# Kernel optimization log

Hardware: AMD Instinct MI355X
Metric: run time of the kernel (lower is better)

## Reference

```python
import jax, jax.numpy as jnp
import numpy as np

DEPTH = 6

def sparsemax(z):
    # sparsemax over last axis (Martins & Astudillo 2016)
    z_sorted = -jnp.sort(-z, axis=-1)
    z_cum = jnp.cumsum(z_sorted, axis=-1)
    k = jnp.arange(1, z.shape[-1] + 1, dtype=z.dtype)
    support = k * z_sorted > z_cum - 1.0
    k_sup = jnp.sum(support, axis=-1, keepdims=True).astype(jnp.int32)
    tau_sum = jnp.take_along_axis(z_cum, k_sup - 1, axis=-1)
    tau = (tau_sum - 1.0) / k_sup.astype(z.dtype)
    return jnp.maximum(z - tau, 0.0)

def sparsemoid(x):
    return jnp.clip(0.5 * x + 0.5, 0.0, 1.0)

def make_bin_codes(depth):
    indices = jnp.arange(2 ** depth)
    offsets = 2 ** jnp.arange(depth)
    bin_codes = ((indices[None, :] // offsets[:, None]) % 2).astype(jnp.float32)
    return jnp.stack([bin_codes, 1.0 - bin_codes], axis=-1)  # [depth, 2^depth, 2]

def odste_forward(x, fsl, esl, thr, lt, resp, codes):
    # x: [B,J,D]; fsl: [n,t,J]; esl: [n,t,J,D]; thr/lt: [n,t]; resp: [n,c,D,2^t]
    fs = sparsemax(fsl)                               # [n,t,J]
    es = sparsemax(esl)                               # [n,t,J,D]
    sel = jnp.einsum('bjd,ntj->bntd', x, fs)          # feature selection
    sel = sel * jnp.sum(es, axis=2)[None]             # einsum 'bntd,ntjd->bntd'
    tl = (sel - thr[None, :, :, None]) * jnp.exp(-lt)[None, :, :, None]
    tl = jnp.stack([-tl, tl], axis=-1)                # [b,n,t,d,2]
    bins = sparsemoid(tl)
    bm = jnp.einsum('bntds,tcs->bntdc', bins, codes)  # [b,n,t,d,c]
    rw = jnp.prod(bm, axis=2)                         # [b,n,d,c]
    return jnp.einsum('bnds,ncds->bnd', rw, resp)     # [b,n,d]


def setup_inputs() -> dict:
    key = jax.random.key(0)
    B, D, n, t, c_tree = 64, 32, 128, DEPTH, 1
    Js = [64, 192, 320]
    ks = jax.random.split(key, 1 + 5 * len(Js))
    inp = {'x': jax.random.normal(ks[0], (B, Js[0], D), dtype=jnp.float32)}
    for i, J in enumerate(Js):
        k0, k1, k2, k3, k4 = ks[1 + 5 * i:6 + 5 * i]
        inp[f'fsl_{i}'] = jax.random.uniform(k0, (n, t, J), dtype=jnp.float32)
        inp[f'esl_{i}'] = jax.random.normal(k1, (n, t, J, D), dtype=jnp.float32)
        inp[f'thr_{i}'] = jax.random.normal(k2, (n, t), dtype=jnp.float32)
        inp[f'lt_{i}'] = jax.random.normal(k3, (n, t), dtype=jnp.float32)
        inp[f'resp_{i}'] = jax.random.normal(k4, (n, c_tree, D, 2 ** t), dtype=jnp.float32)
    return inp


def reference(x, fsl_0, esl_0, thr_0, lt_0, resp_0,
              fsl_1, esl_1, thr_1, lt_1, resp_1,
              fsl_2, esl_2, thr_2, lt_2, resp_2):
    codes = make_bin_codes(DEPTH)
    layers = [(fsl_0, esl_0, thr_0, lt_0, resp_0),
              (fsl_1, esl_1, thr_1, lt_1, resp_1),
              (fsl_2, esl_2, thr_2, lt_2, resp_2)]
    for fsl, esl, thr, lt, resp in layers:
        h = odste_forward(x, fsl, esl, thr, lt, resp, codes)
        x = jnp.concatenate([x, h], axis=1)
    return x
```

## Files before the change

### kernel.cpp

```cpp
#include <hip/hip_runtime.h>

#define OUT_COLS 448
#define OUT_STRIDE (OUT_COLS * 32)
#define NTREES 128
#define TDEPTH 6
#define NT (NTREES * TDEPTH)
#define DD 32
#define BB 64
#define PADW 64

template <int CTRL, int RMASK = 0xf, bool BC = true>
__device__ __forceinline__ float dppf(float v) {
    return __int_as_float(
        __builtin_amdgcn_update_dpp(0, __float_as_int(v), CTRL, RMASK, 0xf, BC));
}

__device__ __forceinline__ float wred64(float x) {
    x += dppf<0x111>(x);
    x += dppf<0x112>(x);
    x += dppf<0x114>(x);
    x += dppf<0x118>(x);
    x += __int_as_float(__builtin_amdgcn_update_dpp(0, __float_as_int(x), 0x142, 0xa, 0xf, false));
    x += __int_as_float(__builtin_amdgcn_update_dpp(0, __float_as_int(x), 0x143, 0xc, 0xf, false));
    return __int_as_float(__builtin_amdgcn_readlane(__float_as_int(x), 63));
}

template <int J>
__device__ __forceinline__ void fs_row(const float* __restrict__ zr, int lane,
                                       int* __restrict__ fj, float* __restrict__ fv,
                                       int* __restrict__ fcnt_p) {
    constexpr int T = J / 64;
    float z[T];
    #pragma unroll
    for (int t = 0; t < T; ++t) z[t] = zr[t * 64 + lane];
    float sp = 0.f;
    #pragma unroll
    for (int t = 0; t < T; ++t) sp += z[t];
    float k = (float)J;
    float tau = (wred64(sp) - 1.f) / k;
    #pragma unroll 1
    for (int it = 0; it < 64; ++it) {
        float s2 = 0.f, c2 = 0.f;
        #pragma unroll
        for (int t = 0; t < T; ++t) {
            bool g = z[t] > tau;
            s2 += g ? z[t] : 0.f;
            c2 += g ? 1.f : 0.f;
        }
        float S2 = wred64(s2);
        float K2 = wred64(c2);
        if (K2 == k) break;
        k = K2;
        tau = (S2 - 1.f) / K2;
    }
    unsigned long long below = (1ull << lane) - 1ull;
    int base = 0;
    #pragma unroll
    for (int t = 0; t < T; ++t) {
        bool sup = z[t] > tau;
        unsigned long long m = __ballot(sup);
        int pos = base + __popcll(m & below);
        if (sup && pos < PADW) { fj[pos] = t * 64 + lane; fv[pos] = z[t] - tau; }
        base += __popcll(m);
    }
    int cnt = base < PADW ? base : PADW;
    for (int i = cnt + lane; i < PADW; i += 64) { fj[i] = 0; fv[i] = 0.f; }
    if (lane == 0) *fcnt_p = cnt;
}

template <int S>
__device__ __forceinline__ void bstep(float* a, int lane) {
    constexpr int half = 16 >> S;
    bool up = ((lane >> S) & 1) != 0;
    #pragma unroll
    for (int q = 0; q < half; ++q) {
        float send = up ? a[q] : a[half + q];
        float recv;
        if constexpr (S == 0)      recv = dppf<0xB1>(send);
        else if constexpr (S == 1) recv = dppf<0x4E>(send);
        else recv = __int_as_float(__builtin_amdgcn_ds_swizzle(
                        __float_as_int(send), ((1 << S) << 10) | 0x1F));
        float keep = up ? a[half + q] : a[q];
        a[q] = keep + recv;
    }
}

__global__ __launch_bounds__(256)
void prep_kernel(const float* __restrict__ x,
                 const float* __restrict__ f0, const float* __restrict__ f1,
                 const float* __restrict__ f2,
                 const float* __restrict__ e0, const float* __restrict__ e1,
                 const float* __restrict__ e2,
                 int* __restrict__ fjp, float* __restrict__ fvp, int* __restrict__ fcnt,
                 float* __restrict__ part, float* __restrict__ out) {
    int w = blockIdx.x * 4 + (threadIdx.x >> 6);
    int lane = threadIdx.x & 63;

    if (w < 512) {
        const float4* x4 = (const float4*)x;
        float4* o4 = (float4*)out;
        int g = w * 64 + lane;
        int b = g >> 9, r = g & 511;
        o4[(size_t)b * (OUT_STRIDE / 4) + r] = x4[g];
        return;
    }
    w -= 512;
    if (w < 3 * NT) {
        if (w < NT) {
            fs_row<64>(f0 + (size_t)w * 64, lane,
                       fjp + (size_t)w * PADW, fvp + (size_t)w * PADW, fcnt + w);
        } else if (w < 2 * NT) {
            int r = w - NT;
            fs_row<192>(f1 + (size_t)r * 192, lane,
                        fjp + (size_t)(NT + r) * PADW, fvp + (size_t)(NT + r) * PADW,
                        fcnt + NT + r);
        } else {
            int r = w - 2 * NT;
            fs_row<320>(f2 + (size_t)r * 320, lane,
                        fjp + (size_t)(2 * NT + r) * PADW, fvp + (size_t)(2 * NT + r) * PADW,
                        fcnt + 2 * NT + r);
        }
        return;
    }
    w -= 3 * NT;
    const float* esl; int row, chunk, J; size_t grow;
    if (w < NT)          { esl = e0; row = w; chunk = 0; J = 64; grow = (size_t)row; }
    else if (w < 4 * NT) { int q = w - NT; esl = e1; row = q / 3; chunk = q - row * 3; J = 192; grow = (size_t)(NT + row); }
    else                 { int q = w - 4 * NT; esl = e2; row = q / 5; chunk = q - row * 5; J = 320; grow = (size_t)(2 * NT + row); }

    const float4* zp4 = (const float4*)(esl + ((size_t)row * J + chunk * 64 + lane) * 32);
    float z[32];
    #pragma unroll
    for (int i = 0; i < 8; ++i) {
        float4 v = zp4[i];
        z[4 * i] = v.x; z[4 * i + 1] = v.y; z[4 * i + 2] = v.z; z[4 * i + 3] = v.w;
    }
    float mx = z[0];
    #pragma unroll
    for (int i = 1; i < 32; ++i) mx = fmaxf(mx, z[i]);
    float tau = mx - 1.0f;
    int kprev = -1;
    #pragma unroll 1
    for (int it = 0; it < 40; ++it) {
        float s0 = 0.f, s1 = 0.f, s2 = 0.f, s3 = 0.f;
        int k0 = 0, k1 = 0, k2 = 0, k3 = 0;
        #pragma unroll
        for (int i = 0; i < 8; ++i) {
            bool g0 = z[4 * i]     > tau; s0 += g0 ? z[4 * i]     : 0.f; k0 += g0;
            bool g1 = z[4 * i + 1] > tau; s1 += g1 ? z[4 * i + 1] : 0.f; k1 += g1;
            bool g2 = z[4 * i + 2] > tau; s2 += g2 ? z[4 * i + 2] : 0.f; k2 += g2;
            bool g3 = z[4 * i + 3] > tau; s3 += g3 ? z[4 * i + 3] : 0.f; k3 += g3;
        }
        float S = (s0 + s1) + (s2 + s3);
        int k = (k0 + k1) + (k2 + k3);
        bool chg = (k != kprev);
        kprev = k;
        tau = (S - 1.0f) / (float)k;
        if (__ballot(chg) == 0ull) break;
    }
    #pragma unroll
    for (int i = 0; i < 32; ++i) z[i] = fmaxf(z[i] - tau, 0.f);
    bstep<0>(z, lane);
    bstep<1>(z, lane);
    bstep<2>(z, lane);
    bstep<3>(z, lane);
    bstep<4>(z, lane);
    z[0] += __shfl_xor(z[0], 32, 64);
    if (lane < 32) {
        int d = ((lane & 1) << 4) | ((lane & 2) << 2) | (lane & 4)
              | ((lane & 8) >> 2) | ((lane & 16) >> 4);
        part[(grow * 5 + chunk) * 32 + d] = z[0];
    }
}

__global__ __launch_bounds__(256)
void main_kernel(const int* __restrict__ fjp, const float* __restrict__ fvp,
                 const int* __restrict__ fcnt, const float* __restrict__ partL, int nch,
                 const float* __restrict__ thr, const float* __restrict__ lt,
                 const float* __restrict__ resp,
                 float* __restrict__ out, int colOff) {
    int n = blockIdx.x;
    int tid = threadIdx.x;
    __shared__ int   s_j[TDEPTH][PADW];
    __shared__ float s_v[TDEPTH][PADW];
    __shared__ float s_resp[DD][65];
    __shared__ float s_ess[TDEPTH][DD];
    __shared__ float s_thr[TDEPTH], s_elt[TDEPTH];
    __shared__ int   s_cnt[TDEPTH];

    for (int i = tid; i < TDEPTH * PADW; i += 256) {
        int t = i >> 6, p = i & 63;
        size_t g = (size_t)(n * TDEPTH + t) * PADW + p;
        s_j[t][p] = fjp[g];
        s_v[t][p] = fvp[g];
    }
    for (int i = tid; i < DD * 64; i += 256) {
        s_resp[i >> 6][i & 63] = resp[(size_t)n * (DD * 64) + i];
    }
    if (tid < TDEPTH * DD) {
        int t = tid >> 5, d = tid & 31;
        float e = 0.f;
        #pragma unroll
        for (int c = 0; c < 5; ++c)
            if (c < nch) e += partL[((size_t)(n * TDEPTH + t) * 5 + c) * 32 + d];
        s_ess[t][d] = e;
    }
    if (tid < TDEPTH) {
        int r = n * TDEPTH + tid;
        s_thr[tid] = thr[r];
        s_elt[tid] = expf(-lt[r]);
        s_cnt[tid] = fcnt[r];
    }
    __syncthreads();

    int b = blockIdx.y * 8 + (tid >> 5);
    int d = tid & 31;
    const float* xb = out + (size_t)b * OUT_STRIDE;

    float sv[TDEPTH];
    #pragma unroll
    for (int t = 0; t < TDEPTH; ++t) {
        float acc = 0.f;
        int c16 = (s_cnt[t] + 15) & ~15;
        for (int p = 0; p < c16; p += 16) {
            int jj[16]; float vv[16];
            #pragma unroll
            for (int q = 0; q < 16; ++q) { jj[q] = s_j[t][p + q]; vv[q] = s_v[t][p + q]; }
            #pragma unroll
            for (int q = 0; q < 16; ++q) acc += xb[jj[q] * 32 + d] * vv[q];
        }
        float sel = acc * s_ess[t][d];
        float tlv = (sel - s_thr[t]) * s_elt[t];
        sv[t] = fminf(fmaxf(0.5f * tlv + 0.5f, 0.f), 1.f);
    }

    float pr[64];
    pr[0] = sv[0];
    pr[1] = 1.f - sv[0];
    #pragma unroll
    for (int t = 1; t < TDEPTH; ++t) {
        const int len = 1 << t;
        float f1 = 1.f - sv[t];
        #pragma unroll
        for (int c = 0; c < 64; ++c) {
            if (c < len) {
                int cc = len - 1 - c;
                pr[cc + len] = pr[cc] * f1;
                pr[cc]       = pr[cc] * sv[t];
            }
        }
    }
    float o = 0.f;
    #pragma unroll
    for (int c = 0; c < 64; ++c) o += pr[c] * s_resp[d][c];
    out[(size_t)b * OUT_STRIDE + (size_t)(colOff + n) * DD + d] = o;
}

extern "C" void kernel_launch(void* const* d_in, const int* in_sizes, int n_in,
                              void* d_out, int out_size, void* d_ws, size_t ws_size,
                              hipStream_t stream) {
    const float* x = (const float*)d_in[0];
    float* out = (float*)d_out;

    const size_t NPAD = (size_t)3 * NT * PADW;
    char* ws = (char*)d_ws;
    int*   fjp  = (int*)(ws);
    float* fvp  = (float*)(ws + NPAD * 4);
    int*   fcnt = (int*)(ws + 2 * NPAD * 4);
    float* part = (float*)(ws + 2 * NPAD * 4 + 16384);

    prep_kernel<<<9728 / 4, 256, 0, stream>>>(
        x,
        (const float*)d_in[1], (const float*)d_in[6], (const float*)d_in[11],
        (const float*)d_in[2], (const float*)d_in[7], (const float*)d_in[12],
        fjp, fvp, fcnt, part, out);

    const int nchs[3] = {1, 3, 5};
    int colOff = 64;
    for (int L = 0; L < 3; ++L) {
        const float* thr  = (const float*)d_in[3 + 5 * L];
        const float* lt   = (const float*)d_in[4 + 5 * L];
        const float* resp = (const float*)d_in[5 + 5 * L];
        main_kernel<<<dim3(NTREES, 8), 256, 0, stream>>>(
            fjp + (size_t)L * NT * PADW, fvp + (size_t)L * NT * PADW,
            fcnt + L * NT, part + (size_t)L * NT * 5 * 32, nchs[L],
            thr, lt, resp, out, colOff);
        colOff += NTREES;
    }
}
```

Measured before the change: 58.29 us.

## Factor leaf-probability product into two 8-wide halves and cut register pressure

The 64 leaf probabilities are no longer expanded into a 64-register array. The response dot product is factored into an outer product of two 8-element partial products (depths 0-2 and 3-5), which cuts both register use and multiplies. The gather loop drops from 16-wide staged index/value loads to 8-wide direct loads, and launch bounds now request 6 waves per EU to raise occupancy. The trade-offs are less memory-level parallelism per thread in the gather and slightly different floating-point rounding order.

```diff
diff --git a/kernel.cpp b/kernel.cpp
--- a/kernel.cpp
+++ b/kernel.cpp
@@ -173,7 +173,7 @@
     }
 }
 
-__global__ __launch_bounds__(256)
+__global__ __launch_bounds__(256, 6)
 void main_kernel(const int* __restrict__ fjp, const float* __restrict__ fvp,
                  const int* __restrict__ fcnt, const float* __restrict__ partL, int nch,
                  const float* __restrict__ thr, const float* __restrict__ lt,
@@ -221,38 +221,43 @@
     #pragma unroll
     for (int t = 0; t < TDEPTH; ++t) {
         float acc = 0.f;
-        int c16 = (s_cnt[t] + 15) & ~15;
-        for (int p = 0; p < c16; p += 16) {
-            int jj[16]; float vv[16];
+        int c8 = (s_cnt[t] + 7) & ~7;
+        for (int p = 0; p < c8; p += 8) {
             #pragma unroll
-            for (int q = 0; q < 16; ++q) { jj[q] = s_j[t][p + q]; vv[q] = s_v[t][p + q]; }
-            #pragma unroll
-            for (int q = 0; q < 16; ++q) acc += xb[jj[q] * 32 + d] * vv[q];
+            for (int q = 0; q < 8; ++q)
+                acc += xb[s_j[t][p + q] * 32 + d] * s_v[t][p + q];
         }
         float sel = acc * s_ess[t][d];
         float tlv = (sel - s_thr[t]) * s_elt[t];
         sv[t] = fminf(fmaxf(0.5f * tlv + 0.5f, 0.f), 1.f);
     }
 
-    float pr[64];
-    pr[0] = sv[0];
-    pr[1] = 1.f - sv[0];
-    #pragma unroll
-    for (int t = 1; t < TDEPTH; ++t) {
-        const int len = 1 << t;
-        float f1 = 1.f - sv[t];
-        #pragma unroll
-        for (int c = 0; c < 64; ++c) {
-            if (c < len) {
-                int cc = len - 1 - c;
-                pr[cc + len] = pr[cc] * f1;
-                pr[cc]       = pr[cc] * sv[t];
-            }
-        }
+    float A[8], Bv[8];
+    {
+        float a0 = sv[0], a1 = 1.f - sv[0];
+        float b0 = sv[1], b1 = 1.f - sv[1];
+        float c0 = sv[2], c1 = 1.f - sv[2];
+        A[0] = a0 * b0 * c0; A[1] = a1 * b0 * c0;
+        A[2] = a0 * b1 * c0; A[3] = a1 * b1 * c0;
+        A[4] = a0 * b0 * c1; A[5] = a1 * b0 * c1;
+        A[6] = a0 * b1 * c1; A[7] = a1 * b1 * c1;
+        float d0 = sv[3], d1 = 1.f - sv[3];
+        float e0 = sv[4], e1 = 1.f - sv[4];
+        float f0 = sv[5], f1 = 1.f - sv[5];
+        Bv[0] = d0 * e0 * f0; Bv[1] = d1 * e0 * f0;
+        Bv[2] = d0 * e1 * f0; Bv[3] = d1 * e1 * f0;
+        Bv[4] = d0 * e0 * f1; Bv[5] = d1 * e0 * f1;
+        Bv[6] = d0 * e1 * f1; Bv[7] = d1 * e1 * f1;
     }
     float o = 0.f;
     #pragma unroll
-    for (int c = 0; c < 64; ++c) o += pr[c] * s_resp[d][c];
+    for (int c2 = 0; c2 < 8; ++c2) {
+        float inner = 0.f;
+        #pragma unroll
+        for (int c1 = 0; c1 < 8; ++c1)
+            inner += A[c1] * s_resp[d][c1 + 8 * c2];
+        o += Bv[c2] * inner;
+    }
     out[(size_t)b * OUT_STRIDE + (size_t)(colOff + n) * DD + d] = o;
 }
 
```

Measured after the change: 58.88 us. About the same (+1.0%).
